# Kernel tuning notes

Hardware: AMD Instinct MI355X
Metric: run time of the kernel (lower is better)

Reference implementation:

```python
import jax, jax.numpy as jnp
import numpy as np
from jax import lax

N, IC, OC, K, SDIM, H, W = 16, 512, 512, 3, 512, 32, 32
PAD, STRIDE, LR = 1, 1, 1.0
WEIGHT_SCALER = 1.0 / np.sqrt(IC * K * K) * LR   # equalized-lr conv scale
FC_SCALER = 1.0 / np.sqrt(SDIM) * LR             # equalized-lr fc scale


def setup_inputs() -> dict:
    key = jax.random.key(0)
    k1, k2, k3 = jax.random.split(key, 3)
    x = jax.random.normal(k1, (N, IC, H, W), dtype=jnp.float32)
    style = jax.random.normal(k2, (N, SDIM), dtype=jnp.float32)
    weight = jax.random.normal(k3, (OC, IC, K, K), dtype=jnp.float32)  # std = 1/lr = 1
    fc_weight = jax.random.normal(jax.random.fold_in(key, 10), (IC, SDIM), dtype=jnp.float32)
    fc_bias = jnp.zeros((IC,), dtype=jnp.float32)
    return {"x": x, "style": style, "weight": weight,
            "fc_weight": fc_weight, "fc_bias": fc_bias}


def reference(x, style, weight, fc_weight, fc_bias):
    # EqualizedFullyConnect + AddChannelwiseBias, then +1 -> modulation rates [N, iC]
    mod = jnp.einsum('ns,cs->nc', style, fc_weight) * FC_SCALER + fc_bias * LR + 1.0
    # modulated per-sample weight [N, oC, iC, kH, kW]
    w = WEIGHT_SCALER * weight[None] * mod[:, None, :, None, None]
    # demodulate: rsqrt of sum of squares over (iC, kH, kW)
    demod = lax.rsqrt(jnp.sum(w * w, axis=(2, 3, 4)) + 1e-8)  # [N, oC]
    w = w * demod[:, :, None, None, None]
    # grouped conv with groups=N == per-sample conv: vmap over batch
    def conv1(xi, wi):
        # xi: [iC,H,W], wi: [oC,iC,kH,kW]
        return lax.conv_general_dilated(
            xi[None], wi, window_strides=(STRIDE, STRIDE),
            padding=((PAD, PAD), (PAD, PAD)),
            dimension_numbers=('NCHW', 'OIHW', 'NCHW'))[0]
    out = jax.vmap(conv1)(x, w)  # [N, oC, H, W]
    return out
```

## Files before the change

### kernel.cpp

```cpp
#include <hip/hip_runtime.h>
#include <hip/hip_bf16.h>

#define N_    16
#define IC_   512
#define OC_   512
#define SDIM_ 512
#define H_    32
#define W_    32
#define HW_   1024

#define FC_SCALER 0.04419417382415922f
#define WS_       0.014731391274719738f
#define WS2_      (1.0f/4608.0f)

typedef __attribute__((__ext_vector_type__(8)))  __bf16 bf16x8;
typedef __attribute__((__ext_vector_type__(16))) float  f32x16;
typedef __attribute__((__ext_vector_type__(4)))  int    i32x4;

typedef __attribute__((address_space(1))) const unsigned int GInt;
typedef __attribute__((address_space(3))) unsigned int LInt;

__device__ __forceinline__ unsigned short f2bf(float f) {
    unsigned int u = __builtin_bit_cast(unsigned int, f);
    unsigned int r = (u + 0x7FFFu + ((u >> 16) & 1u)) >> 16;
    return (unsigned short)r;
}

__global__ void k_mod(const float* __restrict__ style, const float* __restrict__ fcw,
                      const float* __restrict__ fcb, float* __restrict__ mod) {
    int gid = blockIdx.x * blockDim.x + threadIdx.x;
    int wid = gid >> 6, lane = gid & 63;
    if (wid >= N_ * IC_) return;
    int n = wid >> 9, c = wid & 511;
    const float4* sp = (const float4*)(style + n * SDIM_);
    const float4* wp = (const float4*)(fcw + (size_t)c * SDIM_);
    float acc = 0.f;
    for (int i = lane; i < SDIM_ / 4; i += 64) {
        float4 a = sp[i], b = wp[i];
        acc += a.x*b.x + a.y*b.y + a.z*b.z + a.w*b.w;
    }
#pragma unroll
    for (int off = 32; off; off >>= 1) acc += __shfl_xor(acc, off);
    if (lane == 0) mod[wid] = acc * FC_SCALER + fcb[c] + 1.0f;
}

__global__ void k_wprep(const float* __restrict__ w, unsigned short* __restrict__ wt,
                        float* __restrict__ wsq) {
    int tid = blockIdx.x * blockDim.x + threadIdx.x;
    int oc = tid >> 9, ic = tid & 511;
    int og = oc >> 7, ocl = oc & 127;
    int icc = ic >> 6, k6 = ic & 63, ks = k6 >> 3, i8 = k6 & 7;
    float s = 0.f;
#pragma unroll
    for (int t = 0; t < 9; t++) {
        float v = w[(size_t)tid * 9 + t];
        s += v * v;
        size_t off = ((((size_t)t * 4 + og) * 8 + icc) * 8192)
                   + (size_t)ks * 1024 + ocl * 8 + i8;
        wt[off] = f2bf(v);
    }
    wsq[tid] = s;
}

__global__ void k_demod(const float* __restrict__ mod, const float* __restrict__ wsq,
                        float* __restrict__ demod_ws) {
    int gid = blockIdx.x * blockDim.x + threadIdx.x;
    int wid = gid >> 6, lane = gid & 63;
    if (wid >= N_ * OC_) return;
    int n = wid >> 9, oc = wid & 511;
    const float4* mp = (const float4*)(mod + n * IC_);
    const float4* qp = (const float4*)(wsq + (size_t)oc * IC_);
    float acc = 0.f;
    for (int i = lane; i < IC_ / 4; i += 64) {
        float4 m = mp[i], q = qp[i];
        acc += m.x*m.x*q.x + m.y*m.y*q.y + m.z*m.z*q.z + m.w*m.w*q.w;
    }
#pragma unroll
    for (int off = 32; off; off >>= 1) acc += __shfl_xor(acc, off);
    if (lane == 0) {
        float s = WS2_ * acc + 1e-8f;
        demod_ws[wid] = WS_ / sqrtf(s);
    }
}

__global__ void k_premod(const float* __restrict__ x, const float* __restrict__ mod,
                         unsigned short* __restrict__ xm) {
    __shared__ __align__(16) unsigned short t_lds[64][80];
    int bx = blockIdx.x;
    int n = bx >> 7, hwt = (bx >> 3) & 15, ict = bx & 7;
    int hw0 = hwt * 64, ic0 = ict * 64;
    int tid = threadIdx.x, lane = tid & 63, ty = tid >> 6;
#pragma unroll
    for (int jj = 0; jj < 16; jj++) {
        int icl = ty * 16 + jj;
        float v = x[(size_t)(n * IC_ + ic0 + icl) * HW_ + hw0 + lane]
                  * mod[n * IC_ + ic0 + icl];
        t_lds[lane][icl] = f2bf(v);
    }
    __syncthreads();
    int xcol = tid & 31, ks = tid >> 5;
#pragma unroll
    for (int rep = 0; rep < 2; rep++) {
        int hwl = rep * 32 + xcol;
        i32x4 v = *(const i32x4*)&t_lds[hwl][ks * 8];
        int y = (hw0 >> 5) + rep;
        size_t off = ((((size_t)n * 8 + ict) * 32 + y) * 8 + ks) * 256 + xcol * 8;
        *(i32x4*)(xm + off) = v;
    }
}

__global__ __launch_bounds__(256, 1)
void k_conv(const unsigned short* __restrict__ xm, const unsigned short* __restrict__ wt,
            const float* __restrict__ demod_ws, float* __restrict__ out) {
    __shared__ __align__(16) unsigned short xt[2][10 * 2048];
    __shared__ __align__(16) unsigned short wb[2][8192];
    __shared__ __align__(16) float zslot[4];
    __shared__ float s_demod[128];

    int bx = blockIdx.x;
    int octg = bx >> 6, n = (bx >> 2) & 15, spt = bx & 3;
    int oc0 = octg * 128, y0 = spt * 8;
    int tid = threadIdx.x, lane = tid & 63, wid = tid >> 6;
    int l31 = lane & 31, lhi = lane >> 5;

    if (tid < 128) s_demod[tid] = demod_ws[n * OC_ + oc0 + tid];
    if (tid == 0) { zslot[0] = 0.f; zslot[1] = 0.f; zslot[2] = 0.f; zslot[3] = 0.f; }
    if (spt == 0) {
        i32x4 z = {};
        *(i32x4*)&xt[0][tid * 8] = z;
        *(i32x4*)&xt[1][tid * 8] = z;
    }
    if (spt == 3) {
        i32x4 z = {};
        *(i32x4*)&xt[0][9 * 2048 + tid * 8] = z;
        *(i32x4*)&xt[1][9 * 2048 + tid * 8] = z;
    }

    const unsigned short* xsrc_n = xm + (size_t)n * (8 * 32 * 2048);

    auto stage_x = [&](int buf, int icc) {
        for (int wl = wid; wl < 40; wl += 4) {
            int rr = wl >> 2, j = wl & 3;
            int y = y0 - 1 + rr;
            if ((unsigned)y < 32u) {
                const unsigned short* g =
                    xsrc_n + ((size_t)icc * 32 + y) * 2048 + j * 512 + lane * 8;
                unsigned short* l = &xt[buf][rr * 2048 + j * 512];
                __builtin_amdgcn_global_load_lds((GInt*)g, (LInt*)l, 16, 0, 0);
            }
        }
    };
    auto stage_w = [&](int buf, int tap, int icc) {
        const unsigned short* wsrcc = wt + (((size_t)tap * 4 + octg) * 8 + icc) * 8192;
        for (int wl = wid; wl < 16; wl += 4) {
            const unsigned short* g = wsrcc + wl * 512 + lane * 8;
            unsigned short* l = &wb[buf][wl * 512];
            __builtin_amdgcn_global_load_lds((GInt*)g, (LInt*)l, 16, 0, 0);
        }
    };

    f32x16 acc[4][2] = {};

    stage_x(0, 0);
    stage_w(0, 0, 0);
    __syncthreads();

    int xb = 0, wcur = 0;
#pragma unroll 1
    for (int icc = 0; icc < 8; icc++) {
#pragma unroll 1
        for (int t = 0; t < 9; t++) {
            if (t == 0 && icc < 7) stage_x(xb ^ 1, icc + 1);
            if (t < 8)              stage_w(wcur ^ 1, t + 1, icc);
            else if (icc < 7)       stage_w(wcur ^ 1, 0, icc + 1);

            int dy = t / 3, dx = t % 3;
            const unsigned short* wbp = wb[wcur];
            const unsigned short* xtp = xt[xb];
#pragma unroll
            for (int kk = 0; kk < 4; kk++) {
                int kslot = kk * 2 + lhi;
                bf16x8 af[4], bfr[2];
#pragma unroll
                for (int fo = 0; fo < 4; fo++)
                    af[fo] = *(const bf16x8*)(wbp + kslot * 1024 + (fo * 32 + l31) * 8);
#pragma unroll
                for (int fs = 0; fs < 2; fs++) {
                    int rr = wid * 2 + fs + dy;
                    unsigned cp = (unsigned)(l31 + dx) - 1u;
                    const unsigned short* p = (cp < 32u)
                        ? (xtp + rr * 2048 + kslot * 256 + cp * 8)
                        : (const unsigned short*)zslot;
                    bfr[fs] = *(const bf16x8*)p;
                }
#pragma unroll
                for (int fo = 0; fo < 4; fo++)
#pragma unroll
                    for (int fs = 0; fs < 2; fs++)
                        acc[fo][fs] = __builtin_amdgcn_mfma_f32_32x32x16_bf16(
                            af[fo], bfr[fs], acc[fo][fs], 0, 0, 0);
            }
            __syncthreads();
            wcur ^= 1;
        }
        xb ^= 1;
    }

#pragma unroll
    for (int fo = 0; fo < 4; fo++) {
#pragma unroll
        for (int fs = 0; fs < 2; fs++) {
            int y = y0 + wid * 2 + fs;
#pragma unroll
            for (int r = 0; r < 16; r++) {
                int row = (r & 3) + 8 * (r >> 2) + 4 * lhi;
                int ocl = fo * 32 + row;
                float v = acc[fo][fs][r] * s_demod[ocl];
                out[((size_t)(n * OC_ + oc0 + ocl) * H_ + y) * W_ + l31] = v;
            }
        }
    }
}

extern "C" void kernel_launch(void* const* d_in, const int* in_sizes, int n_in,
                              void* d_out, int out_size, void* d_ws, size_t ws_size,
                              hipStream_t stream) {
    const float* x      = (const float*)d_in[0];
    const float* style  = (const float*)d_in[1];
    const float* weight = (const float*)d_in[2];
    const float* fcw    = (const float*)d_in[3];
    const float* fcb    = (const float*)d_in[4];
    float* out = (float*)d_out;

    char* ws = (char*)d_ws;
    float*          mod   = (float*)ws;
    float*          demod = (float*)(ws + 32768);
    float*          wsq   = (float*)(ws + 65536);
    unsigned short* wtb   = (unsigned short*)(ws + 65536 + 1048576);
    unsigned short* xmb   = (unsigned short*)(ws + 65536 + 1048576 + 4718592);

    k_mod   <<<2048, 256, 0, stream>>>(style, fcw, fcb, mod);
    k_wprep <<<1024, 256, 0, stream>>>(weight, wtb, wsq);
    k_demod <<<2048, 256, 0, stream>>>(mod, wsq, demod);
    k_premod<<<2048, 256, 0, stream>>>(x, mod, xmb);
    k_conv  <<<256,  256, 0, stream>>>(xmb, wtb, demod, out);
}
```

Baseline: 118.3 us.

## Triple-buffer weight tiles with vmcnt waits and a 2x2 warp tile layout

Weight staging in the conv kernel moves from a double buffer to a triple buffer, prefetching two taps ahead. The per-tap __syncthreads is replaced by explicit s_waitcnt vmcnt counts plus s_barrier, and the tap loop is fully unrolled. Out-of-bounds x rows are loaded into a trash LDS buffer, so every wave issues a fixed number of loads and the counts stay predictable. Warps are rearranged from a 1x4 split to a 2x2 split over output-channel and row, which changes the per-warp A/B fragment reuse, and MFMA sections get s_setprio. The hand-counted vmcnt values are fragile and need more LDS.

Result: faster. 105.7 us (-10.6%).

```diff
diff --git a/kernel.cpp b/kernel.cpp
--- a/kernel.cpp
+++ b/kernel.cpp
@@ -19,6 +19,10 @@
 
 typedef __attribute__((address_space(1))) const unsigned int GInt;
 typedef __attribute__((address_space(3))) unsigned int LInt;
+
+#define WAIT4()  asm volatile("s_waitcnt vmcnt(4)"  ::: "memory")
+#define WAIT14() asm volatile("s_waitcnt vmcnt(14)" ::: "memory")
+#define WAIT0()  asm volatile("s_waitcnt vmcnt(0)"  ::: "memory")
 
 __device__ __forceinline__ unsigned short f2bf(float f) {
     unsigned int u = __builtin_bit_cast(unsigned int, f);
@@ -113,7 +117,8 @@
 void k_conv(const unsigned short* __restrict__ xm, const unsigned short* __restrict__ wt,
             const float* __restrict__ demod_ws, float* __restrict__ out) {
     __shared__ __align__(16) unsigned short xt[2][10 * 2048];
-    __shared__ __align__(16) unsigned short wb[2][8192];
+    __shared__ __align__(16) unsigned short wb[3][8192];
+    __shared__ __align__(16) unsigned short trash[512];
     __shared__ __align__(16) float zslot[4];
     __shared__ float s_demod[128];
 
@@ -122,9 +127,12 @@
     int oc0 = octg * 128, y0 = spt * 8;
     int tid = threadIdx.x, lane = tid & 63, wid = tid >> 6;
     int l31 = lane & 31, lhi = lane >> 5;
+    int wr = wid >> 1, wc = wid & 1;
 
     if (tid < 128) s_demod[tid] = demod_ws[n * OC_ + oc0 + tid];
-    if (tid == 0) { zslot[0] = 0.f; zslot[1] = 0.f; zslot[2] = 0.f; zslot[3] = 0.f; }
+    __builtin_amdgcn_sched_barrier(0);
+
+    if (tid == 0) { i32x4 z = {}; *(i32x4*)zslot = z; }
     if (spt == 0) {
         i32x4 z = {};
         *(i32x4*)&xt[0][tid * 8] = z;
@@ -140,81 +148,94 @@
 
     auto stage_x = [&](int buf, int icc) {
         for (int wl = wid; wl < 40; wl += 4) {
-            int rr = wl >> 2, j = wl & 3;
+            int rr = wl >> 2, q = wl & 3;
             int y = y0 - 1 + rr;
-            if ((unsigned)y < 32u) {
-                const unsigned short* g =
-                    xsrc_n + ((size_t)icc * 32 + y) * 2048 + j * 512 + lane * 8;
-                unsigned short* l = &xt[buf][rr * 2048 + j * 512];
-                __builtin_amdgcn_global_load_lds((GInt*)g, (LInt*)l, 16, 0, 0);
-            }
+            int yc = y < 0 ? 0 : (y > 31 ? 31 : y);
+            bool oob = (unsigned)y >= 32u;
+            const unsigned short* g =
+                xsrc_n + ((size_t)icc * 32 + yc) * 2048 + q * 512 + lane * 8;
+            unsigned short* l = oob ? (unsigned short*)trash
+                                    : &xt[buf][rr * 2048 + q * 512];
+            __builtin_amdgcn_global_load_lds((GInt*)g, (LInt*)l, 16, 0, 0);
         }
     };
-    auto stage_w = [&](int buf, int tap, int icc) {
+    auto stage_w = [&](int slot, int tap, int icc) {
         const unsigned short* wsrcc = wt + (((size_t)tap * 4 + octg) * 8 + icc) * 8192;
-        for (int wl = wid; wl < 16; wl += 4) {
+#pragma unroll
+        for (int k = 0; k < 4; k++) {
+            int wl = wid + k * 4;
             const unsigned short* g = wsrcc + wl * 512 + lane * 8;
-            unsigned short* l = &wb[buf][wl * 512];
+            unsigned short* l = &wb[slot][wl * 512];
             __builtin_amdgcn_global_load_lds((GInt*)g, (LInt*)l, 16, 0, 0);
         }
     };
 
-    f32x16 acc[4][2] = {};
+    f32x16 acc[2][4] = {};
 
     stage_x(0, 0);
     stage_w(0, 0, 0);
-    __syncthreads();
-
-    int xb = 0, wcur = 0;
+    stage_w(1, 1, 0);
+    asm volatile("s_waitcnt lgkmcnt(0)" ::: "memory");
+
+    int xb = 0;
 #pragma unroll 1
     for (int icc = 0; icc < 8; icc++) {
-#pragma unroll 1
+#pragma unroll
         for (int t = 0; t < 9; t++) {
+            if (t == 1 || t == 2) { if (icc < 7) WAIT14(); else WAIT4(); }
+            else if (icc == 7 && t == 8) WAIT0();
+            else WAIT4();
+            __builtin_amdgcn_s_barrier();
+            {
+                int tt = t + 2;
+                int wicc = icc + (tt >= 9);
+                int wtap = tt >= 9 ? tt - 9 : tt;
+                if (wicc < 8) stage_w((t + 2) % 3, wtap, wicc);
+            }
             if (t == 0 && icc < 7) stage_x(xb ^ 1, icc + 1);
-            if (t < 8)              stage_w(wcur ^ 1, t + 1, icc);
-            else if (icc < 7)       stage_w(wcur ^ 1, 0, icc + 1);
-
-            int dy = t / 3, dx = t % 3;
-            const unsigned short* wbp = wb[wcur];
+
+            const int dy = t / 3, dx = t % 3;
+            const unsigned short* wbp = wb[t % 3];
             const unsigned short* xtp = xt[xb];
+            int colbase = l31 + dx - 1;
+            bool oobc = (unsigned)colbase >= 32u;
 #pragma unroll
             for (int kk = 0; kk < 4; kk++) {
-                int kslot = kk * 2 + lhi;
-                bf16x8 af[4], bfr[2];
-#pragma unroll
-                for (int fo = 0; fo < 4; fo++)
-                    af[fo] = *(const bf16x8*)(wbp + kslot * 1024 + (fo * 32 + l31) * 8);
-#pragma unroll
-                for (int fs = 0; fs < 2; fs++) {
-                    int rr = wid * 2 + fs + dy;
-                    unsigned cp = (unsigned)(l31 + dx) - 1u;
-                    const unsigned short* p = (cp < 32u)
-                        ? (xtp + rr * 2048 + kslot * 256 + cp * 8)
-                        : (const unsigned short*)zslot;
+                int ks = kk * 2 + lhi;
+                bf16x8 af[2], bfr[4];
+#pragma unroll
+                for (int fo = 0; fo < 2; fo++)
+                    af[fo] = *(const bf16x8*)(wbp + ks * 1024 + (wr * 64 + fo * 32 + l31) * 8);
+#pragma unroll
+                for (int fs = 0; fs < 4; fs++) {
+                    int rr = wc * 4 + fs + dy;
+                    const unsigned short* p = oobc
+                        ? (const unsigned short*)zslot
+                        : (xtp + rr * 2048 + ks * 256 + colbase * 8);
                     bfr[fs] = *(const bf16x8*)p;
                 }
-#pragma unroll
-                for (int fo = 0; fo < 4; fo++)
-#pragma unroll
-                    for (int fs = 0; fs < 2; fs++)
+                __builtin_amdgcn_s_setprio(1);
+#pragma unroll
+                for (int fo = 0; fo < 2; fo++)
+#pragma unroll
+                    for (int fs = 0; fs < 4; fs++)
                         acc[fo][fs] = __builtin_amdgcn_mfma_f32_32x32x16_bf16(
                             af[fo], bfr[fs], acc[fo][fs], 0, 0, 0);
+                __builtin_amdgcn_s_setprio(0);
             }
-            __syncthreads();
-            wcur ^= 1;
         }
         xb ^= 1;
     }
 
 #pragma unroll
-    for (int fo = 0; fo < 4; fo++) {
-#pragma unroll
-        for (int fs = 0; fs < 2; fs++) {
-            int y = y0 + wid * 2 + fs;
+    for (int fo = 0; fo < 2; fo++) {
+#pragma unroll
+        for (int fs = 0; fs < 4; fs++) {
+            int y = y0 + wc * 4 + fs;
 #pragma unroll
             for (int r = 0; r < 16; r++) {
                 int row = (r & 3) + 8 * (r >> 2) + 4 * lhi;
-                int ocl = fo * 32 + row;
+                int ocl = wr * 64 + fo * 32 + row;
                 float v = acc[fo][fs][r] * s_demod[ocl];
                 out[((size_t)(n * OC_ + oc0 + ocl) * H_ + y) * W_ + l31] = v;
             }
```
